# Optimization experiments

Measured on AMD Instinct MI355X. Metric: run time of the kernel, lower is better.

Reference implementation:

```python
import jax, jax.numpy as jnp
import numpy as np

# priors from init_kwargs
PRIOR_PI = 0.5
PRIOR_S1 = 1.0
PRIOR_S2 = 0.0025
LOG_SQRT_2PI = 0.5 * np.log(2.0 * np.pi).astype(np.float32)


def _normal_logprob(x, sigma):
    # Normal(0, sigma).log_prob(x)
    return -0.5 * (x / sigma) ** 2 - jnp.log(sigma) - LOG_SQRT_2PI


def _mixture_logprob_sum(x, pi, sigma1, sigma2):
    # log(pi * N(x;0,s1) + (1-pi) * N(x;0,s2)).sum(), as in the torch code
    p1 = jnp.exp(_normal_logprob(x, sigma1))
    p2 = jnp.exp(_normal_logprob(x, sigma2))
    return jnp.log(pi * p1 + (1.0 - pi) * p2).sum()


def _sample(pi, rho1, rho2, eps, gum):
    # ScaleMixtureGaussian_VarPost.sample(): gumbel-max over (pi, 1-pi)
    sigma1 = jnp.log1p(jnp.exp(rho1))
    sigma2 = jnp.log1p(jnp.exp(rho2))
    x = jnp.stack((pi, 1.0 - pi), axis=-1)          # [..., 2]
    mode = jnp.argmax(x + gum, axis=-1).astype(pi.dtype)  # [...]
    return mode * sigma1 * eps + (1.0 - mode) * sigma2 * eps


def setup_inputs() -> dict:
    key = jax.random.key(0)
    ks = jax.random.split(key, 12)
    OUT, IN, B = 8192, 4096, 128
    f32 = jnp.float32
    u_w = jax.random.uniform(ks[0], (OUT, IN, 2), dtype=f32, minval=1e-6, maxval=1.0 - 1e-6)
    u_b = jax.random.uniform(ks[1], (OUT, 2), dtype=f32, minval=1e-6, maxval=1.0 - 1e-6)
    return {
        "x": jax.random.normal(ks[2], (B, IN), dtype=f32),
        "w_pi": jax.random.uniform(ks[3], (OUT, IN), dtype=f32),
        "w_rho1": 0.1 * jax.random.normal(ks[4], (OUT, IN), dtype=f32),
        "w_rho2": 0.1 * jax.random.normal(ks[5], (OUT, IN), dtype=f32),
        "b_pi": jax.random.uniform(ks[6], (OUT,), dtype=f32),
        "b_rho1": 0.1 * jax.random.normal(ks[7], (OUT,), dtype=f32),
        "b_rho2": 0.1 * jax.random.normal(ks[8], (OUT,), dtype=f32),
        "eps_w": jax.random.normal(ks[9], (OUT, IN), dtype=f32),
        "eps_b": jax.random.normal(ks[10], (OUT,), dtype=f32),
        "gum_w": -jnp.log(-jnp.log(u_w)),  # Gumbel(0,1)
        "gum_b": -jnp.log(-jnp.log(u_b)),
    }


def reference(x, w_pi, w_rho1, w_rho2, b_pi, b_rho1, b_rho2, eps_w, eps_b, gum_w, gum_b):
    weight = _sample(w_pi, w_rho1, w_rho2, eps_w, gum_w)   # [OUT, IN]
    bias = _sample(b_pi, b_rho1, b_rho2, eps_b, gum_b)     # [OUT]

    log_prior = (_mixture_logprob_sum(weight, PRIOR_PI, PRIOR_S1, PRIOR_S2)
                 + _mixture_logprob_sum(bias, PRIOR_PI, PRIOR_S1, PRIOR_S2))

    sig_w1 = jnp.log1p(jnp.exp(w_rho1))
    sig_w2 = jnp.log1p(jnp.exp(w_rho2))
    sig_b1 = jnp.log1p(jnp.exp(b_rho1))
    sig_b2 = jnp.log1p(jnp.exp(b_rho2))
    log_post = (_mixture_logprob_sum(weight, w_pi, sig_w1, sig_w2)
                + _mixture_logprob_sum(bias, b_pi, sig_b1, sig_b2))

    out = x @ weight.T + bias  # F.linear
    return out, log_prior, log_post
```

## Files before the change

kernel.cpp:

```cpp
#include <hip/hip_runtime.h>

#define OUTN 8192
#define INN  4096
#define BN   128

namespace {

typedef __attribute__((ext_vector_type(8))) short bf16x8;
typedef __attribute__((ext_vector_type(4))) float f32x4;

struct alignas(16) f4 { float v[4]; };
struct alignas(8)  h4 { short v[4]; };

constexpr float C_HLOG2PI = 0.91893853f;

__device__ __forceinline__ short f2bf(float f) {
    unsigned u = __float_as_uint(f);
    u += 0x7fffu + ((u >> 16) & 1u);
    return (short)(u >> 16);
}

__device__ __forceinline__ float prior_lp(float w) {
    float lp1 = -0.5f * w * w - C_HLOG2PI;
    float a   = w * 400.0f;
    float lp2 = -0.5f * a * a + 5.0725261f;
    return __logf(0.5f * __expf(lp1) + 0.5f * __expf(lp2));
}
__device__ __forceinline__ float post_lp(float w, float pi_, float s1, float ls1,
                                         float s2, float ls2) {
    float u1  = __fdividef(w, s1);
    float u2  = __fdividef(w, s2);
    float lq1 = -0.5f * u1 * u1 - ls1 - C_HLOG2PI;
    float lq2 = -0.5f * u2 * u2 - ls2 - C_HLOG2PI;
    return __logf(pi_ * __expf(lq1) + (1.0f - pi_) * __expf(lq2));
}
__device__ __forceinline__ float sample_w(float pi_, float rho1, float rho2, float ep,
                                          float g0, float g1,
                                          float& s1, float& ls1, float& s2, float& ls2) {
    s1  = __logf(1.0f + __expf(rho1));
    s2  = __logf(1.0f + __expf(rho2));
    ls1 = __logf(s1);
    ls2 = __logf(s2);
    bool mode1 = ((1.0f - pi_) + g1) > (pi_ + g0);
    return (mode1 ? s1 : s2) * ep;
}

constexpr int OT = 32;
constexpr int KC = 32;
constexpr int NT = 256;
constexpr int KSTR = 40;

__global__ __launch_bounds__(NT, 4)
void bayes_main(const float* __restrict__ x,
                const float* __restrict__ w_pi,
                const float* __restrict__ w_rho1,
                const float* __restrict__ w_rho2,
                const float* __restrict__ eps_w,
                const float* __restrict__ gum_w,
                const float* __restrict__ bias,
                float* __restrict__ out,
                float* __restrict__ pbuf,
                float* __restrict__ partials,
                int kps, int nsplit)
{
    __shared__ alignas(16) short Wt[OT][KSTR];
    __shared__ alignas(16) short Xs[BN][KSTR];
    __shared__ float red[8];

    const int tid   = threadIdx.x;
    const int split = blockIdx.x >> 8;
    const int tile  = blockIdx.x & 255;
    const int o0    = tile * OT;
    const int k0    = split * kps;
    const int nch   = kps / KC;
    float* outp = (split == 0) ? out : pbuf + (size_t)(split - 1) * ((size_t)BN * OUTN);

    const int c = tid & 7;
    const int r = tid >> 3;

    const size_t wbase = (size_t)(o0 + r) * INN + k0;
    const f4* pi4 = (const f4*)(w_pi   + wbase) + c;
    const f4* r14 = (const f4*)(w_rho1 + wbase) + c;
    const f4* r24 = (const f4*)(w_rho2 + wbase) + c;
    const f4* ep4 = (const f4*)(eps_w  + wbase) + c;
    const f4* gm4 = (const f4*)(gum_w  + 2 * wbase) + 2 * c;
    const f4* xp  = (const f4*)(x + (size_t)r * INN + k0) + c;

    f32x4 acc00 = {0.f,0.f,0.f,0.f}, acc01 = {0.f,0.f,0.f,0.f};
    f32x4 acc10 = {0.f,0.f,0.f,0.f}, acc11 = {0.f,0.f,0.f,0.f};
    float priorAcc = 0.0f, postAcc = 0.0f;

    const int wv_  = tid >> 6;
    const int lane = tid & 63;
    const int lrow = lane & 15;
    const int lgo  = (lane >> 4) * 8;

    f4 vpi = pi4[0], vr1 = r14[0], vr2 = r24[0], vep = ep4[0];
    f4 vga = gm4[0], vgb = gm4[1];
    f4 vx0 = xp[0], vx1 = xp[32768], vx2 = xp[65536], vx3 = xp[98304];

    for (int t = 0; t < nch; ++t) {
        h4 wb;
        #pragma unroll
        for (int i = 0; i < 4; ++i) {
            const f4& g = (i < 2) ? vga : vgb;
            float g0 = g.v[(i & 1) * 2], g1 = g.v[(i & 1) * 2 + 1];
            float pi_ = vpi.v[i], ep = vep.v[i];
            float s1  = __logf(1.0f + __expf(vr1.v[i]));
            float s2  = __logf(1.0f + __expf(vr2.v[i]));
            float ls1 = __logf(s1), ls2 = __logf(s2);
            bool  m1  = ((1.0f - pi_) + g1) > (pi_ + g0);
            float sm  = m1 ? s1 : s2;
            float so  = m1 ? s2 : s1;
            float lsm = m1 ? ls1 : ls2;
            float lso = m1 ? ls2 : ls1;
            float wm  = m1 ? pi_ : 1.0f - pi_;
            float w   = sm * ep;
            wb.v[i] = f2bf(w);
            float wsq = w * w;
            float dlp = 5.9914645f - 79999.5f * wsq;
            priorAcc += -0.5f * wsq - C_HLOG2PI + __logf(0.5f + 0.5f * __expf(dlp));
            float uo   = __fdividef(w, so);
            float epsq = ep * ep;
            float dlq  = 0.5f * (epsq - uo * uo) + (lsm - lso);
            postAcc += -0.5f * epsq - lsm - C_HLOG2PI
                       + __logf(wm + (1.0f - wm) * __expf(dlq));
        }

        __syncthreads();
        *(h4*)&Wt[r][4 * c] = wb;
        {
            h4 xb;
            #pragma unroll
            for (int i = 0; i < 4; ++i) xb.v[i] = f2bf(vx0.v[i]);
            *(h4*)&Xs[r][4 * c] = xb;
            #pragma unroll
            for (int i = 0; i < 4; ++i) xb.v[i] = f2bf(vx1.v[i]);
            *(h4*)&Xs[r + 32][4 * c] = xb;
            #pragma unroll
            for (int i = 0; i < 4; ++i) xb.v[i] = f2bf(vx2.v[i]);
            *(h4*)&Xs[r + 64][4 * c] = xb;
            #pragma unroll
            for (int i = 0; i < 4; ++i) xb.v[i] = f2bf(vx3.v[i]);
            *(h4*)&Xs[r + 96][4 * c] = xb;
        }
        __syncthreads();

        const int tn = (t + 1 < nch) ? t + 1 : 0;
        vpi = pi4[8*tn]; vr1 = r14[8*tn]; vr2 = r24[8*tn]; vep = ep4[8*tn];
        vga = gm4[16*tn]; vgb = gm4[16*tn + 1];
        vx0 = xp[8*tn]; vx1 = xp[8*tn + 32768];
        vx2 = xp[8*tn + 65536]; vx3 = xp[8*tn + 98304];

        bf16x8 a0 = *(const bf16x8*)&Xs[32 * wv_      + lrow][lgo];
        bf16x8 a1 = *(const bf16x8*)&Xs[32 * wv_ + 16 + lrow][lgo];
        bf16x8 b0 = *(const bf16x8*)&Wt[lrow     ][lgo];
        bf16x8 b1 = *(const bf16x8*)&Wt[16 + lrow][lgo];
        acc00 = __builtin_amdgcn_mfma_f32_16x16x32_bf16(a0, b0, acc00, 0, 0, 0);
        acc01 = __builtin_amdgcn_mfma_f32_16x16x32_bf16(a0, b1, acc01, 0, 0, 0);
        acc10 = __builtin_amdgcn_mfma_f32_16x16x32_bf16(a1, b0, acc10, 0, 0, 0);
        acc11 = __builtin_amdgcn_mfma_f32_16x16x32_bf16(a1, b1, acc11, 0, 0, 0);
    }

    {
        const int oc = o0 + lrow;
        const int bb = 32 * wv_ + (lane >> 4) * 4;
        const float bv0 = bias ? bias[oc]      : 0.0f;
        const float bv1 = bias ? bias[oc + 16] : 0.0f;
        #pragma unroll
        for (int j = 0; j < 4; ++j) {
            outp[(size_t)(bb      + j) * OUTN + oc     ] = acc00[j] + bv0;
            outp[(size_t)(bb      + j) * OUTN + oc + 16] = acc01[j] + bv1;
            outp[(size_t)(bb + 16 + j) * OUTN + oc     ] = acc10[j] + bv0;
            outp[(size_t)(bb + 16 + j) * OUTN + oc + 16] = acc11[j] + bv1;
        }
    }

    #pragma unroll
    for (int off = 32; off; off >>= 1) {
        priorAcc += __shfl_down(priorAcc, off);
        postAcc  += __shfl_down(postAcc, off);
    }
    if ((tid & 63) == 0) { red[wv_] = priorAcc; red[4 + wv_] = postAcc; }
    __syncthreads();
    if (tid == 0) {
        partials[2*blockIdx.x    ] = red[0] + red[1] + red[2] + red[3];
        partials[2*blockIdx.x + 1] = red[4] + red[5] + red[6] + red[7];
    }
}

__global__ __launch_bounds__(256)
void bayes_bias(const float* __restrict__ b_pi, const float* __restrict__ b_rho1,
                const float* __restrict__ b_rho2, const float* __restrict__ eps_b,
                const float* __restrict__ gum_b,
                float* __restrict__ bias_vals, float* __restrict__ bpart)
{
    __shared__ float red[8];
    const int tid = threadIdx.x;
    const int o = blockIdx.x * 256 + tid;
    float pi_ = b_pi[o], rho1 = b_rho1[o], rho2 = b_rho2[o], ep = eps_b[o];
    float g0 = gum_b[2*o], g1 = gum_b[2*o + 1];
    float s1, ls1, s2, ls2;
    float w = sample_w(pi_, rho1, rho2, ep, g0, g1, s1, ls1, s2, ls2);
    bias_vals[o] = w;
    float pa = prior_lp(w);
    float qa = post_lp(w, pi_, s1, ls1, s2, ls2);
    #pragma unroll
    for (int off = 32; off; off >>= 1) {
        pa += __shfl_down(pa, off);
        qa += __shfl_down(qa, off);
    }
    const int wave = tid >> 6;
    if ((tid & 63) == 0) { red[wave] = pa; red[4 + wave] = qa; }
    __syncthreads();
    if (tid == 0) {
        bpart[2*blockIdx.x    ] = red[0] + red[1] + red[2] + red[3];
        bpart[2*blockIdx.x + 1] = red[4] + red[5] + red[6] + red[7];
    }
}

__global__ __launch_bounds__(256)
void bayes_reduce(float* __restrict__ out, const float* __restrict__ pbuf,
                  const float* __restrict__ bias, int nsplit)
{
    const size_t i = ((size_t)blockIdx.x * 256 + threadIdx.x) * 4;
    const int o = (int)(i & (OUTN - 1));
    f4 a  = *(const f4*)&out[i];
    f4 bq = *(const f4*)&bias[o];
    #pragma unroll 1
    for (int s = 0; s < nsplit - 1; ++s) {
        f4 p = *(const f4*)&pbuf[(size_t)s * ((size_t)BN * OUTN) + i];
        #pragma unroll
        for (int j = 0; j < 4; ++j) a.v[j] += p.v[j];
    }
    #pragma unroll
    for (int j = 0; j < 4; ++j) a.v[j] += bq.v[j];
    *(f4*)&out[i] = a;
}

__global__ void bayes_final(const float* __restrict__ partials, int cnt,
                            float* __restrict__ out_scalars)
{
    const int lane = threadIdx.x;
    double p = 0.0, q = 0.0;
    for (int j = lane; j < cnt; j += 64) {
        p += (double)partials[2*j];
        q += (double)partials[2*j + 1];
    }
    #pragma unroll
    for (int off = 32; off; off >>= 1) {
        p += __shfl_down(p, off);
        q += __shfl_down(q, off);
    }
    if (lane == 0) {
        out_scalars[0] = (float)p;
        out_scalars[1] = (float)q;
    }
}

}

extern "C" void kernel_launch(void* const* d_in, const int* in_sizes, int n_in,
                              void* d_out, int out_size, void* d_ws, size_t ws_size,
                              hipStream_t stream) {
    (void)in_sizes; (void)n_in; (void)out_size;
    const float* x      = (const float*)d_in[0];
    const float* w_pi   = (const float*)d_in[1];
    const float* w_rho1 = (const float*)d_in[2];
    const float* w_rho2 = (const float*)d_in[3];
    const float* b_pi   = (const float*)d_in[4];
    const float* b_rho1 = (const float*)d_in[5];
    const float* b_rho2 = (const float*)d_in[6];
    const float* eps_w  = (const float*)d_in[7];
    const float* eps_b  = (const float*)d_in[8];
    const float* gum_w  = (const float*)d_in[9];
    const float* gum_b  = (const float*)d_in[10];

    float* out = (float*)d_out;
    float* ws  = (float*)d_ws;
    float* bias_vals = ws;
    float* partials  = ws + 8192;
    float* pbuf      = ws + 12288;

    const size_t outElems = (size_t)BN * OUTN;
    int NS = 1;
    if (ws_size >= (12288 + 3 * outElems) * sizeof(float)) NS = 4;
    else if (ws_size >= (12288 + 1 * outElems) * sizeof(float)) NS = 2;

    float* bpart = partials + 2 * 256 * NS;
    const int cnt = 256 * NS + 32;

    if (NS == 1) {
        bayes_bias<<<32, 256, 0, stream>>>(b_pi, b_rho1, b_rho2, eps_b, gum_b,
                                           bias_vals, bpart);
        bayes_main<<<256, NT, 0, stream>>>(x, w_pi, w_rho1, w_rho2, eps_w, gum_w,
                                           bias_vals, out, pbuf, partials, INN, 1);
    } else {
        bayes_main<<<256 * NS, NT, 0, stream>>>(x, w_pi, w_rho1, w_rho2, eps_w, gum_w,
                                                nullptr, out, pbuf, partials,
                                                INN / NS, NS);
        bayes_bias<<<32, 256, 0, stream>>>(b_pi, b_rho1, b_rho2, eps_b, gum_b,
                                           bias_vals, bpart);
        bayes_reduce<<<(int)(outElems / 4 / 256), 256, 0, stream>>>(out, pbuf,
                                                                    bias_vals, NS);
    }
    bayes_final<<<1, 64, 0, stream>>>(partials, cnt, out + outElems);
}
```

Measured before the change: 211.2 us.

## Pre-cast x to bf16 once and load MFMA A operands directly from global

Adds a small kernel that converts x to bf16 in workspace once, so the main kernel no longer converts and stages x through shared memory for every output tile. Each wave now loads its bf16x8 A fragments straight from global memory, prefetched one chunk ahead. This cuts LDS usage, which allows launch bounds to rise to 6 blocks per CU. The split-K factor can also go up to 8 when workspace allows, at the cost of more partial buffers to reduce and an extra kernel launch.

After: 273.4 us. 29.5% more time.

```diff
diff --git a/kernel.cpp b/kernel.cpp
--- a/kernel.cpp
+++ b/kernel.cpp
@@ -50,8 +50,21 @@
 constexpr int NT = 256;
 constexpr int KSTR = 40;
 
-__global__ __launch_bounds__(NT, 4)
-void bayes_main(const float* __restrict__ x,
+__global__ __launch_bounds__(256)
+void xcast(const float* __restrict__ x, short* __restrict__ xb)
+{
+    const int i = (blockIdx.x * 256 + threadIdx.x) * 8;
+    f4 a = *(const f4*)&x[i];
+    f4 b = *(const f4*)&x[i + 4];
+    h4 o0, o1;
+    #pragma unroll
+    for (int j = 0; j < 4; ++j) { o0.v[j] = f2bf(a.v[j]); o1.v[j] = f2bf(b.v[j]); }
+    *(h4*)&xb[i]     = o0;
+    *(h4*)&xb[i + 4] = o1;
+}
+
+__global__ __launch_bounds__(NT, 6)
+void bayes_main(const short* __restrict__ xb,
                 const float* __restrict__ w_pi,
                 const float* __restrict__ w_rho1,
                 const float* __restrict__ w_rho2,
@@ -64,7 +77,6 @@
                 int kps, int nsplit)
 {
     __shared__ alignas(16) short Wt[OT][KSTR];
-    __shared__ alignas(16) short Xs[BN][KSTR];
     __shared__ float red[8];
 
     const int tid   = threadIdx.x;
@@ -84,7 +96,6 @@
     const f4* r24 = (const f4*)(w_rho2 + wbase) + c;
     const f4* ep4 = (const f4*)(eps_w  + wbase) + c;
     const f4* gm4 = (const f4*)(gum_w  + 2 * wbase) + 2 * c;
-    const f4* xp  = (const f4*)(x + (size_t)r * INN + k0) + c;
 
     f32x4 acc00 = {0.f,0.f,0.f,0.f}, acc01 = {0.f,0.f,0.f,0.f};
     f32x4 acc10 = {0.f,0.f,0.f,0.f}, acc11 = {0.f,0.f,0.f,0.f};
@@ -95,9 +106,13 @@
     const int lrow = lane & 15;
     const int lgo  = (lane >> 4) * 8;
 
+    const short* xrow0 = xb + (size_t)(32 * wv_ + lrow) * INN + k0 + lgo;
+    const short* xrow1 = xrow0 + 16 * INN;
+
     f4 vpi = pi4[0], vr1 = r14[0], vr2 = r24[0], vep = ep4[0];
     f4 vga = gm4[0], vgb = gm4[1];
-    f4 vx0 = xp[0], vx1 = xp[32768], vx2 = xp[65536], vx3 = xp[98304];
+    bf16x8 a0 = *(const bf16x8*)(xrow0);
+    bf16x8 a1 = *(const bf16x8*)(xrow1);
 
     for (int t = 0; t < nch; ++t) {
         h4 wb;
@@ -129,37 +144,21 @@
 
         __syncthreads();
         *(h4*)&Wt[r][4 * c] = wb;
-        {
-            h4 xb;
-            #pragma unroll
-            for (int i = 0; i < 4; ++i) xb.v[i] = f2bf(vx0.v[i]);
-            *(h4*)&Xs[r][4 * c] = xb;
-            #pragma unroll
-            for (int i = 0; i < 4; ++i) xb.v[i] = f2bf(vx1.v[i]);
-            *(h4*)&Xs[r + 32][4 * c] = xb;
-            #pragma unroll
-            for (int i = 0; i < 4; ++i) xb.v[i] = f2bf(vx2.v[i]);
-            *(h4*)&Xs[r + 64][4 * c] = xb;
-            #pragma unroll
-            for (int i = 0; i < 4; ++i) xb.v[i] = f2bf(vx3.v[i]);
-            *(h4*)&Xs[r + 96][4 * c] = xb;
-        }
         __syncthreads();
 
         const int tn = (t + 1 < nch) ? t + 1 : 0;
         vpi = pi4[8*tn]; vr1 = r14[8*tn]; vr2 = r24[8*tn]; vep = ep4[8*tn];
         vga = gm4[16*tn]; vgb = gm4[16*tn + 1];
-        vx0 = xp[8*tn]; vx1 = xp[8*tn + 32768];
-        vx2 = xp[8*tn + 65536]; vx3 = xp[8*tn + 98304];
-
-        bf16x8 a0 = *(const bf16x8*)&Xs[32 * wv_      + lrow][lgo];
-        bf16x8 a1 = *(const bf16x8*)&Xs[32 * wv_ + 16 + lrow][lgo];
+        bf16x8 a0n = *(const bf16x8*)(xrow0 + 32 * tn);
+        bf16x8 a1n = *(const bf16x8*)(xrow1 + 32 * tn);
+
         bf16x8 b0 = *(const bf16x8*)&Wt[lrow     ][lgo];
         bf16x8 b1 = *(const bf16x8*)&Wt[16 + lrow][lgo];
         acc00 = __builtin_amdgcn_mfma_f32_16x16x32_bf16(a0, b0, acc00, 0, 0, 0);
         acc01 = __builtin_amdgcn_mfma_f32_16x16x32_bf16(a0, b1, acc01, 0, 0, 0);
         acc10 = __builtin_amdgcn_mfma_f32_16x16x32_bf16(a1, b0, acc10, 0, 0, 0);
         acc11 = __builtin_amdgcn_mfma_f32_16x16x32_bf16(a1, b1, acc11, 0, 0, 0);
+        a0 = a0n; a1 = a1n;
     }
 
     {
@@ -271,8 +270,8 @@
     const float* b_pi   = (const float*)d_in[4];
     const float* b_rho1 = (const float*)d_in[5];
     const float* b_rho2 = (const float*)d_in[6];
+    const float* eps_b  = (const float*)d_in[8];
     const float* eps_w  = (const float*)d_in[7];
-    const float* eps_b  = (const float*)d_in[8];
     const float* gum_w  = (const float*)d_in[9];
     const float* gum_b  = (const float*)d_in[10];
 
@@ -280,23 +279,27 @@
     float* ws  = (float*)d_ws;
     float* bias_vals = ws;
     float* partials  = ws + 8192;
-    float* pbuf      = ws + 12288;
+    short* xb        = (short*)(ws + 16384);
+    float* pbuf      = ws + 540672;
 
     const size_t outElems = (size_t)BN * OUTN;
     int NS = 1;
-    if (ws_size >= (12288 + 3 * outElems) * sizeof(float)) NS = 4;
-    else if (ws_size >= (12288 + 1 * outElems) * sizeof(float)) NS = 2;
+    if      (ws_size >= (540672 + 7 * outElems) * sizeof(float)) NS = 8;
+    else if (ws_size >= (540672 + 3 * outElems) * sizeof(float)) NS = 4;
+    else if (ws_size >= (540672 + 1 * outElems) * sizeof(float)) NS = 2;
 
     float* bpart = partials + 2 * 256 * NS;
     const int cnt = 256 * NS + 32;
+
+    xcast<<<(BN * INN) / (256 * 8), 256, 0, stream>>>(x, xb);
 
     if (NS == 1) {
         bayes_bias<<<32, 256, 0, stream>>>(b_pi, b_rho1, b_rho2, eps_b, gum_b,
                                            bias_vals, bpart);
-        bayes_main<<<256, NT, 0, stream>>>(x, w_pi, w_rho1, w_rho2, eps_w, gum_w,
+        bayes_main<<<256, NT, 0, stream>>>(xb, w_pi, w_rho1, w_rho2, eps_w, gum_w,
                                            bias_vals, out, pbuf, partials, INN, 1);
     } else {
-        bayes_main<<<256 * NS, NT, 0, stream>>>(x, w_pi, w_rho1, w_rho2, eps_w, gum_w,
+        bayes_main<<<256 * NS, NT, 0, stream>>>(xb, w_pi, w_rho1, w_rho2, eps_w, gum_w,
                                                 nullptr, out, pbuf, partials,
                                                 INN / NS, NS);
         bayes_bias<<<32, 256, 0, stream>>>(b_pi, b_rho1, b_rho2, eps_b, gum_b,
```
